# Kernel optimization log

Measured on AMD Instinct MI355X. Metric: run time of the kernel, lower is better.

The kernel has to match this reference:

```python
import jax, jax.numpy as jnp
import numpy as np
from jax import lax

T, B = 128, 256          # rollout length x num envs
H, W, C = 7, 7, 3        # minigrid obs
HID = 128                # lstm hidden
NA = 7                   # actions
NFLAT = 64 * 4 * 4       # conv flatten (7->6->5->4)


def setup_inputs() -> dict:
    key = jax.random.key(0)
    ks = jax.random.split(key, 20)
    N = T * B
    obs = jax.random.randint(ks[0], (N, H, W, C), 0, 11).astype(jnp.float32)
    done = (jax.random.uniform(ks[1], (N,)) < 0.05).astype(jnp.float32)
    h0 = jnp.zeros((1, B, HID), jnp.float32)
    c0 = jnp.zeros((1, B, HID), jnp.float32)
    s = 0.1
    conv1_w = jax.random.normal(ks[2], (16, C, 2, 2)) * s
    conv1_b = jnp.zeros((16,), jnp.float32)
    conv2_w = jax.random.normal(ks[3], (32, 16, 2, 2)) * s
    conv2_b = jnp.zeros((32,), jnp.float32)
    conv3_w = jax.random.normal(ks[4], (64, 32, 2, 2)) * s
    conv3_b = jnp.zeros((64,), jnp.float32)
    w_ih = jax.random.normal(ks[5], (4 * HID, NFLAT)) * 0.03
    w_hh = jax.random.normal(ks[6], (4 * HID, HID)) * 0.08
    b_ih = jnp.zeros((4 * HID,), jnp.float32)
    b_hh = jnp.zeros((4 * HID,), jnp.float32)
    actor_w = jax.random.normal(ks[7], (NA, HID)) * 0.01
    actor_b = jnp.zeros((NA,), jnp.float32)
    critic_w = jax.random.normal(ks[8], (1, HID)) * 0.08
    critic_b = jnp.zeros((1,), jnp.float32)
    return dict(obs=obs, done=done, h0=h0, c0=c0,
                conv1_w=conv1_w, conv1_b=conv1_b,
                conv2_w=conv2_w, conv2_b=conv2_b,
                conv3_w=conv3_w, conv3_b=conv3_b,
                w_ih=w_ih, w_hh=w_hh, b_ih=b_ih, b_hh=b_hh,
                actor_w=actor_w, actor_b=actor_b,
                critic_w=critic_w, critic_b=critic_b)


def _conv(x, w, b):
    # x: [N, Cin, h, w], w: [Cout, Cin, 2, 2], VALID, stride 1
    y = lax.conv_general_dilated(x, w, (1, 1), 'VALID',
                                 dimension_numbers=('NCHW', 'OIHW', 'NCHW'))
    return jax.nn.relu(y + b[None, :, None, None])


def reference(obs, done, h0, c0,
              conv1_w, conv1_b, conv2_w, conv2_b, conv3_w, conv3_b,
              w_ih, w_hh, b_ih, b_hh, actor_w, actor_b, critic_w, critic_b):
    N = obs.shape[0]
    x = jnp.transpose(obs, (0, 3, 1, 2))            # NHWC -> NCHW
    x = _conv(x, conv1_w, conv1_b)
    x = _conv(x, conv2_w, conv2_b)
    x = _conv(x, conv3_w, conv3_b)
    feat = x.reshape(N, -1)                          # [T*B, 1024]

    nb = h0.shape[1]
    xs = feat.reshape(-1, nb, feat.shape[-1])        # [T, B, 1024]
    ds = done.reshape(-1, nb)                        # [T, B]
    bias = b_ih + b_hh

    def step(carry, inp):
        h, c = carry                                  # [B, HID]
        x_t, d_t = inp
        m = (1.0 - d_t)[:, None]
        h = m * h
        c = m * c
        gates = x_t @ w_ih.T + h @ w_hh.T + bias      # [B, 4*HID]
        i, f, g, o = jnp.split(gates, 4, axis=-1)     # torch gate order i,f,g,o
        i = jax.nn.sigmoid(i)
        f = jax.nn.sigmoid(f)
        g = jnp.tanh(g)
        o = jax.nn.sigmoid(o)
        c = f * c + i * g
        h = o * jnp.tanh(c)
        return (h, c), h

    (hT, cT), hs = lax.scan(step, (h0[0], c0[0]), (xs, ds))
    hid = hs.reshape(N, -1)                           # [T*B, HID]
    logits = hid @ actor_w.T + actor_b                # [T*B, NA]
    value = hid @ critic_w.T + critic_b               # [T*B, 1]
    out = jnp.concatenate([logits, value], axis=-1)   # [T*B, NA+1]
    return out, hT[None], cT[None]
```

## Files before the change

### kernel.cpp

```cpp
#include <hip/hip_runtime.h>
#include <hip/hip_bf16.h>


#define N_IMG   32768
#define T_LEN   128
#define B_ENV   256
#define HID     128

typedef _Float16 f16x8 __attribute__((ext_vector_type(8)));
typedef _Float16 f16x2 __attribute__((ext_vector_type(2)));
typedef float    f32x4 __attribute__((ext_vector_type(4)));
typedef unsigned short ushort8v __attribute__((ext_vector_type(8)));
typedef unsigned short ushort4v __attribute__((ext_vector_type(4)));

__device__ __forceinline__ float sigm_(float x) { return 1.0f / (1.0f + __expf(-x)); }
__device__ __forceinline__ float tanh_(float x) { return 2.0f / (1.0f + __expf(-2.0f * x)) - 1.0f; }

__device__ __forceinline__ unsigned short f2h(float x) {
    _Float16 h = (_Float16)x;
    union { _Float16 h; unsigned short u; } un; un.h = h;
    return un.u;
}

#if defined(__has_builtin)
#if __has_builtin(__builtin_amdgcn_fdot2)
#define HAVE_FDOT2 1
#endif
#endif

__device__ __forceinline__ float dot2_(f16x2 a, f16x2 b, float c) {
#ifdef HAVE_FDOT2
    return __builtin_amdgcn_fdot2(a, b, c, false);
#else
    c = fmaf((float)a[0], (float)b[0], c);
    return fmaf((float)a[1], (float)b[1], c);
#endif
}

#define GLDS16(g, l) __builtin_amdgcn_global_load_lds( \
    (const __attribute__((address_space(1))) unsigned int*)(g), \
    (__attribute__((address_space(3))) unsigned int*)(l), 16, 0, 0)

__global__ void prep_wih(const float* __restrict__ w, unsigned short* __restrict__ wb)
{
    const int idx = blockIdx.x * 256 + threadIdx.x;
    const int n = idx >> 10, kk = idx & 1023;
    const int p = kk >> 6, co = kk & 63;
    wb[idx] = f2h(w[n * 1024 + co * 16 + p]);
}

__global__ void prep_convw(const float* __restrict__ w2, const float* __restrict__ w3,
                           unsigned short* __restrict__ wb2g, unsigned short* __restrict__ wb3g)
{
    const int t = blockIdx.x * 256 + threadIdx.x;
    if (t < 2048) {
        const int j = t & 7, lane = (t >> 3) & 63, f = t >> 9;
        const int ky = f >> 1, ct = f & 1;
        const int k = ((lane >> 4) << 3) + j, kx = k >> 4, ci = k & 15;
        wb2g[t] = f2h(w2[(ct * 16 + (lane & 15)) * 64 + ci * 4 + ky * 2 + kx]);
    } else if (t < 10240) {
        const int u = t - 2048;
        const int j = u & 7, lane = (u >> 3) & 63, f = u >> 9;
        const int ct = f >> 2, pos = f & 3;
        const int ci = ((lane >> 4) << 3) + j;
        wb3g[u] = f2h(w3[(ct * 16 + (lane & 15)) * 128 + ci * 4 + pos]);
    }
}

__global__ void prep_whh16(const float* __restrict__ w_hh, unsigned short* __restrict__ whh16)
{
    const int idx = blockIdx.x * 256 + threadIdx.x;
    whh16[idx] = f2h(w_hh[idx]);
}

__global__ __launch_bounds__(256, 2) void conv_fused(
    const float* __restrict__ obs,
    const float* __restrict__ w1, const float* __restrict__ b1,
    const float* __restrict__ b2, const float* __restrict__ b3,
    const unsigned short* __restrict__ wb2g,
    const unsigned short* __restrict__ wb3g,
    unsigned short* __restrict__ featb)
{
    __shared__ __align__(16) unsigned char u1[25856];
    __shared__ __align__(16) unsigned char u2[33024];
    __shared__ float w1s[192];
    __shared__ float b1s[16];

    float* s_obs = (float*)u1;
    unsigned short* c2s = (unsigned short*)u1;
    unsigned short* c1s = (unsigned short*)u2;
    unsigned short* c3s = (unsigned short*)u2;

    const int tid = threadIdx.x, lane = tid & 63, wv = tid >> 6;
    const int base = blockIdx.x * 16;

    if (tid < 192) w1s[tid] = w1[tid];
    if (tid < 16)  b1s[tid] = b1[tid];
    for (int i = tid; i < 16 * 147; i += 256) {
        const int im = i / 147, r = i - im * 147;
        s_obs[im * 148 + r] = obs[(size_t)(base + im) * 147 + r];
    }
    __syncthreads();

    {
        const int img = tid & 15;
        const float* ob = &s_obs[img * 148];
        for (int p = tid >> 4; p < 36; p += 16) {
            const int py = p / 6, px = p % 6;
            float o[12];
#pragma unroll
            for (int ky = 0; ky < 2; ky++)
#pragma unroll
                for (int kx = 0; kx < 2; kx++)
#pragma unroll
                    for (int cc = 0; cc < 3; cc++)
                        o[cc * 4 + ky * 2 + kx] = ob[((py + ky) * 7 + px + kx) * 3 + cc];
            unsigned short res[16];
#pragma unroll
            for (int ci = 0; ci < 16; ci++) {
                float a = b1s[ci];
#pragma unroll
                for (int q = 0; q < 12; q++) a = fmaf(o[q], w1s[ci * 12 + q], a);
                res[ci] = f2h(fmaxf(a, 0.0f));
            }
            *(ushort8v*)&c1s[img * 584 + p * 16]     = *(ushort8v*)&res[0];
            *(ushort8v*)&c1s[img * 584 + p * 16 + 8] = *(ushort8v*)&res[8];
        }
    }
    __syncthreads();

    {
        const int ct = wv & 1, par = wv >> 1;
        const int img = lane & 15, kq = lane >> 4;
        f16x8 wA[2];
        wA[0] = *(const f16x8*)&wb2g[(0 + ct) * 512 + lane * 8];
        wA[1] = *(const f16x8*)&wb2g[(2 + ct) * 512 + lane * 8];
        const float4 b2v = *(const float4*)&b2[ct * 16 + kq * 4];
#pragma unroll 2
        for (int p = par; p < 25; p += 2) {
            const int py = p / 5, px = p % 5;
            f32x4 acc = {0.f, 0.f, 0.f, 0.f};
#pragma unroll
            for (int ky = 0; ky < 2; ky++) {
                const int pix = (py + ky) * 6 + px + (kq >> 1);
                const f16x8 bv = *(const f16x8*)&c1s[img * 584 + pix * 16 + (kq & 1) * 8];
                acc = __builtin_amdgcn_mfma_f32_16x16x32_f16(wA[ky], bv, acc, 0, 0, 0);
            }
            unsigned short r4[4];
            r4[0] = f2h(fmaxf(acc[0] + b2v.x, 0.0f));
            r4[1] = f2h(fmaxf(acc[1] + b2v.y, 0.0f));
            r4[2] = f2h(fmaxf(acc[2] + b2v.z, 0.0f));
            r4[3] = f2h(fmaxf(acc[3] + b2v.w, 0.0f));
            *(ushort4v*)&c2s[img * 808 + p * 32 + ct * 16 + kq * 4] = *(ushort4v*)&r4[0];
        }
    }
    __syncthreads();

    {
        const int ct = wv;
        const int img = lane & 15, kq = lane >> 4;
        f16x8 wA3[4];
#pragma unroll
        for (int pos = 0; pos < 4; pos++)
            wA3[pos] = *(const f16x8*)&wb3g[(ct * 4 + pos) * 512 + lane * 8];
        const float4 b3v = *(const float4*)&b3[ct * 16 + kq * 4];
#pragma unroll 4
        for (int p = 0; p < 16; p++) {
            const int py = p >> 2, px = p & 3;
            f32x4 acc = {0.f, 0.f, 0.f, 0.f};
#pragma unroll
            for (int pos = 0; pos < 4; pos++) {
                const int pix = (py + (pos >> 1)) * 5 + px + (pos & 1);
                const f16x8 bv = *(const f16x8*)&c2s[img * 808 + pix * 32 + kq * 8];
                acc = __builtin_amdgcn_mfma_f32_16x16x32_f16(wA3[pos], bv, acc, 0, 0, 0);
            }
            unsigned short r4[4];
            r4[0] = f2h(fmaxf(acc[0] + b3v.x, 0.0f));
            r4[1] = f2h(fmaxf(acc[1] + b3v.y, 0.0f));
            r4[2] = f2h(fmaxf(acc[2] + b3v.z, 0.0f));
            r4[3] = f2h(fmaxf(acc[3] + b3v.w, 0.0f));
            *(ushort4v*)&c3s[img * 1032 + p * 64 + ct * 16 + kq * 4] = *(ushort4v*)&r4[0];
        }
    }
    __syncthreads();

#pragma unroll
    for (int i = 0; i < 8; i++) {
        const int gi = i * 2048 + tid * 8;
        const int img = gi >> 10, flat = gi & 1023;
        *(ushort8v*)&featb[(size_t)(base + img) * 1024 + flat] =
            *(const ushort8v*)&c3s[img * 1032 + flat];
    }
}

__global__ __launch_bounds__(256, 2) void gemm_xproj_mfma(
    const unsigned short* __restrict__ A,
    const unsigned short* __restrict__ W,
    float* __restrict__ C)
{
    __shared__ unsigned short As[128 * 32];
    __shared__ unsigned short Bs[128 * 32];

    const int tid  = threadIdx.x;
    const int bx = blockIdx.x & 3;
    const int by = blockIdx.x >> 2;
    const int m0 = by * 128, n0 = bx * 128;
    const int lane = tid & 63, wave = tid >> 6;
    const int wm = (wave >> 1) * 64, wn = (wave & 1) * 64;
    const int srow = tid >> 2, sseg = tid & 3;

    const unsigned short* Ag = A + (size_t)(m0 + srow) * 1024 + sseg * 8;
    const unsigned short* Wg = W + (size_t)(n0 + srow) * 1024 + sseg * 8;

    f32x4 acc[4][4];
#pragma unroll
    for (int i = 0; i < 4; i++)
#pragma unroll
        for (int j = 0; j < 4; j++) acc[i][j] = (f32x4){0.f, 0.f, 0.f, 0.f};

    const int fr = lane & 15, fq = lane >> 4;

    for (int k0 = 0; k0 < 1024; k0 += 32) {
        __syncthreads();
        GLDS16(Ag + k0,             (char*)As + tid * 16);
        GLDS16(Ag + k0 + 64 * 1024, (char*)As + tid * 16 + 4096);
        GLDS16(Wg + k0,             (char*)Bs + tid * 16);
        GLDS16(Wg + k0 + 64 * 1024, (char*)Bs + tid * 16 + 4096);
        __syncthreads();

        f16x8 af[4], bfv[4];
#pragma unroll
        for (int i = 0; i < 4; i++)
            af[i] = *(const f16x8*)&As[(wm + i * 16 + fr) * 32 + fq * 8];
#pragma unroll
        for (int j = 0; j < 4; j++)
            bfv[j] = *(const f16x8*)&Bs[(wn + j * 16 + fr) * 32 + fq * 8];
#pragma unroll
        for (int i = 0; i < 4; i++)
#pragma unroll
            for (int j = 0; j < 4; j++)
                acc[i][j] = __builtin_amdgcn_mfma_f32_16x16x32_f16(af[i], bfv[j], acc[i][j], 0, 0, 0);
    }

    const int cr = fq * 4, cc = fr;
#pragma unroll
    for (int i = 0; i < 4; i++) {
#pragma unroll
        for (int j = 0; j < 4; j++) {
            float* cp = &C[(size_t)(m0 + wm + i * 16 + cr) * 512 + (n0 + wn + j * 16 + cc)];
#pragma unroll
            for (int r = 0; r < 4; r++)
                cp[(size_t)r * 512] = acc[i][j][r];
        }
    }
}

__global__ __launch_bounds__(1024, 4) void lstm_dot2(
    const float* __restrict__ xproj, const float* __restrict__ done,
    const float* __restrict__ h0, const float* __restrict__ c0,
    const unsigned short* __restrict__ whh16,
    const float* __restrict__ b_ih, const float* __restrict__ b_hh,
    float* __restrict__ hid, float* __restrict__ out)
{
    const int b   = blockIdx.x;
    const int tid = threadIdx.x;
    const int j   = tid >> 1;
    const int hf  = tid & 1;

    __shared__ __align__(16) _Float16 h_s[HID];
    __shared__ float a_s[512];

    f16x8 w8[8];
    {
        const unsigned short* wrow = whh16 + (size_t)j * 128 + hf * 64;
#pragma unroll
        for (int i = 0; i < 8; i++) w8[i] = *(const f16x8*)&wrow[i * 8];
    }
    const float bias = b_ih[j] + b_hh[j];

    float h = 0.0f, c = 0.0f;
    if (tid < HID) { h = h0[b * HID + tid]; c = c0[b * HID + tid]; }

    float xp   = xproj[(size_t)b * 512 + j];
    float dcur = done[b];

    for (int t = 0; t < T_LEN; t++) {
        if (tid < HID) {
            const float m = 1.0f - dcur;
            h *= m; c *= m;
            h_s[tid] = (_Float16)h;
        }
        __syncthreads();

        const int tn = (t + 1 < T_LEN) ? t + 1 : t;
        const float xpn = xproj[((size_t)tn * B_ENV + b) * 512 + j];
        const float dnn = done[tn * B_ENV + b];

        float a0 = 0.f, a1 = 0.f, a2 = 0.f, a3 = 0.f;
#pragma unroll
        for (int i = 0; i < 8; i++) {
            const f16x8 hv = *(const f16x8*)&h_s[hf * 64 + i * 8];
            a0 = dot2_(__builtin_shufflevector(w8[i], w8[i], 0, 1),
                       __builtin_shufflevector(hv,    hv,    0, 1), a0);
            a1 = dot2_(__builtin_shufflevector(w8[i], w8[i], 2, 3),
                       __builtin_shufflevector(hv,    hv,    2, 3), a1);
            a2 = dot2_(__builtin_shufflevector(w8[i], w8[i], 4, 5),
                       __builtin_shufflevector(hv,    hv,    4, 5), a2);
            a3 = dot2_(__builtin_shufflevector(w8[i], w8[i], 6, 7),
                       __builtin_shufflevector(hv,    hv,    6, 7), a3);
        }
        float g = (a0 + a1) + (a2 + a3);
        g += __shfl_xor(g, 1);
        g += bias + xp;

        const float a = (j >= 256 && j < 384) ? tanh_(g) : sigm_(g);
        if (hf == 0) a_s[j] = a;
        __syncthreads();

        if (tid < HID) {
            const float ig = a_s[tid], fg = a_s[tid + 128];
            const float gg = a_s[tid + 256], og = a_s[tid + 384];
            c = fmaf(fg, c, ig * gg);
            h = og * tanh_(c);
            hid[((size_t)t * B_ENV + b) * HID + tid] = h;
        }

        xp   = xpn;
        dcur = dnn;
    }

    if (tid < HID) {
        out[262144 + b * HID + tid] = h;
        out[294912 + b * HID + tid] = c;
    }
}

__global__ __launch_bounds__(256, 2) void heads_kernel(
    const float* __restrict__ hid,
    const float* __restrict__ aw, const float* __restrict__ ab,
    const float* __restrict__ cw, const float* __restrict__ cb,
    float* __restrict__ out)
{
    __shared__ float hs[32 * 129];
    __shared__ float ws[8 * 130];
    __shared__ float bs[8];

    const int tid = threadIdx.x;
    const int n0 = blockIdx.x * 32;

    for (int i = tid; i < 1024; i += 256) {
        const int r = i >> 7, k = i & 127;
        ws[r * 130 + k] = (r < 7) ? aw[r * 128 + k] : cw[k];
    }
    if (tid < 8) bs[tid] = (tid < 7) ? ab[tid] : cb[0];
    for (int i = tid; i < 4096; i += 256) {
        const int r = i >> 7, k = i & 127;
        hs[r * 129 + k] = hid[(size_t)(n0 + r) * 128 + k];
    }
    __syncthreads();

    const int r = tid >> 3, jj = tid & 7;
    float acc = bs[jj];
    const float* hp = &hs[r * 129];
    const float* wp = &ws[jj * 130];
#pragma unroll
    for (int k = 0; k < 128; k++) acc = fmaf(hp[k], wp[k], acc);
    out[(size_t)(n0 + r) * 8 + jj] = acc;
}

extern "C" void kernel_launch(void* const* d_in, const int* in_sizes, int n_in,
                              void* d_out, int out_size, void* d_ws, size_t ws_size,
                              hipStream_t stream)
{
    (void)in_sizes; (void)n_in; (void)out_size; (void)ws_size;

    const float* obs  = (const float*)d_in[0];
    const float* done = (const float*)d_in[1];
    const float* h0   = (const float*)d_in[2];
    const float* c0   = (const float*)d_in[3];
    const float* w1   = (const float*)d_in[4];
    const float* b1   = (const float*)d_in[5];
    const float* w2   = (const float*)d_in[6];
    const float* b2   = (const float*)d_in[7];
    const float* w3   = (const float*)d_in[8];
    const float* b3   = (const float*)d_in[9];
    const float* w_ih = (const float*)d_in[10];
    const float* w_hh = (const float*)d_in[11];
    const float* b_ih = (const float*)d_in[12];
    const float* b_hh = (const float*)d_in[13];
    const float* aw   = (const float*)d_in[14];
    const float* ab   = (const float*)d_in[15];
    const float* cw   = (const float*)d_in[16];
    const float* cb   = (const float*)d_in[17];
    float* out = (float*)d_out;

    unsigned short* featb = (unsigned short*)d_ws;
    unsigned short* wb    = featb + 33554432ull;
    unsigned short* wb2g  = wb    + 524288ull;
    unsigned short* wb3g  = wb2g  + 2048ull;
    float* xproj = (float*)(wb3g + 8192ull + 2048ull);
    float* hid   = xproj + 16777216ull;
    unsigned short* whh16 = (unsigned short*)(hid + 4194304ull);

    prep_wih<<<2048, 256, 0, stream>>>(w_ih, wb);
    prep_convw<<<40, 256, 0, stream>>>(w2, w3, wb2g, wb3g);
    prep_whh16<<<256, 256, 0, stream>>>(w_hh, whh16);
    conv_fused<<<2048, 256, 0, stream>>>(obs, w1, b1, b2, b3, wb2g, wb3g, featb);
    gemm_xproj_mfma<<<1024, 256, 0, stream>>>(featb, wb, xproj);
    lstm_dot2<<<256, 1024, 0, stream>>>(xproj, done, h0, c0, whh16, b_ih, b_hh, hid, out);
    heads_kernel<<<1024, 256, 0, stream>>>(hid, aw, ab, cw, cb, out);
}
```

Before: 333.0 us.

## Restructure LSTM recurrence with butterfly gate reduction and double-buffered hidden state

The LSTM kernel now uses 512 threads per environment, four per hidden unit. Each thread computes partial dot products for all four gates over a 32-wide slice, and a butterfly of xor shuffles leaves each lane holding one full gate pre-activation. Every thread then computes the cell update redundantly, so the gate activations no longer go through shared memory, and with a double-buffered h only one barrier per timestep is needed instead of two. The W_ih rows are permuted in prep so xproj comes out gate-interleaved per hidden unit, and W_hh is repacked to match. The cost is more registers per thread and redundant transcendental work on every lane.

```diff
diff --git a/kernel.cpp b/kernel.cpp
--- a/kernel.cpp
+++ b/kernel.cpp
@@ -12,6 +12,8 @@
 typedef float    f32x4 __attribute__((ext_vector_type(4)));
 typedef unsigned short ushort8v __attribute__((ext_vector_type(8)));
 typedef unsigned short ushort4v __attribute__((ext_vector_type(4)));
+
+union f16x8_pairs { f16x8 v; f16x2 p[4]; };
 
 __device__ __forceinline__ float sigm_(float x) { return 1.0f / (1.0f + __expf(-x)); }
 __device__ __forceinline__ float tanh_(float x) { return 2.0f / (1.0f + __expf(-2.0f * x)) - 1.0f; }
@@ -44,8 +46,10 @@
 __global__ void prep_wih(const float* __restrict__ w, unsigned short* __restrict__ wb)
 {
     const int idx = blockIdx.x * 256 + threadIdx.x;
-    const int n = idx >> 10, kk = idx & 1023;
+    const int np = idx >> 10, kk = idx & 1023;
     const int p = kk >> 6, co = kk & 63;
+    const int g = np & 3, ci = np >> 2;
+    const int n = g * 128 + ci;
     wb[idx] = f2h(w[n * 1024 + co * 16 + p]);
 }
 
@@ -67,10 +71,13 @@
     }
 }
 
-__global__ void prep_whh16(const float* __restrict__ w_hh, unsigned short* __restrict__ whh16)
+__global__ void prep_whhr(const float* __restrict__ w_hh, unsigned short* __restrict__ whhr)
 {
     const int idx = blockIdx.x * 256 + threadIdx.x;
-    whh16[idx] = f2h(w_hh[idx]);
+    const int thr = idx >> 7, r = idx & 127;
+    const int g = r >> 5, k = r & 31;
+    const int ci = thr >> 2, s = thr & 3;
+    whhr[idx] = f2h(w_hh[(g * 128 + ci) * 128 + s * 32 + k]);
 }
 
 __global__ __launch_bounds__(256, 2) void conv_fused(
@@ -255,83 +262,91 @@
     }
 }
 
-__global__ __launch_bounds__(1024, 4) void lstm_dot2(
+__global__ __launch_bounds__(512, 2) void lstm_bfly(
     const float* __restrict__ xproj, const float* __restrict__ done,
     const float* __restrict__ h0, const float* __restrict__ c0,
-    const unsigned short* __restrict__ whh16,
+    const unsigned short* __restrict__ whhr,
     const float* __restrict__ b_ih, const float* __restrict__ b_hh,
     float* __restrict__ hid, float* __restrict__ out)
 {
     const int b   = blockIdx.x;
     const int tid = threadIdx.x;
-    const int j   = tid >> 1;
-    const int hf  = tid & 1;
-
-    __shared__ __align__(16) _Float16 h_s[HID];
-    __shared__ float a_s[512];
-
-    f16x8 w8[8];
+    const int ci  = tid >> 2;
+    const int s   = tid & 3;
+
+    __shared__ __align__(16) _Float16 hbuf[2][HID];
+
+    f16x8_pairs w[4][4];
     {
-        const unsigned short* wrow = whh16 + (size_t)j * 128 + hf * 64;
-#pragma unroll
-        for (int i = 0; i < 8; i++) w8[i] = *(const f16x8*)&wrow[i * 8];
-    }
-    const float bias = b_ih[j] + b_hh[j];
-
-    float h = 0.0f, c = 0.0f;
-    if (tid < HID) { h = h0[b * HID + tid]; c = c0[b * HID + tid]; }
-
-    float xp   = xproj[(size_t)b * 512 + j];
+        const unsigned short* wp = whhr + (size_t)tid * 128;
+#pragma unroll
+        for (int g = 0; g < 4; g++)
+#pragma unroll
+            for (int i = 0; i < 4; i++)
+                w[g][i].v = *(const f16x8*)&wp[g * 32 + i * 8];
+    }
+    const float bias_l = b_ih[s * 128 + ci] + b_hh[s * 128 + ci];
+
+    float c = c0[b * HID + ci];
+    float h = h0[b * HID + ci];
     float dcur = done[b];
 
+    if (tid < HID)
+        hbuf[0][tid] = (_Float16)(h0[b * HID + tid] * (1.0f - dcur));
+
+    float xq = bias_l + xproj[(size_t)b * 512 + ci * 4 + s];
+    __syncthreads();
+
+    int p = 0;
     for (int t = 0; t < T_LEN; t++) {
-        if (tid < HID) {
-            const float m = 1.0f - dcur;
-            h *= m; c *= m;
-            h_s[tid] = (_Float16)h;
-        }
+        const int tn = (t + 1 < T_LEN) ? t + 1 : t;
+        const float xqn = bias_l + xproj[((size_t)tn * B_ENV + b) * 512 + ci * 4 + s];
+        const float dnn = done[tn * B_ENV + b];
+
+        f16x8_pairs hv[4];
+#pragma unroll
+        for (int i = 0; i < 4; i++)
+            hv[i].v = *(const f16x8*)&hbuf[p][s * 32 + i * 8];
+
+        float a0 = (s == 0) ? xq : 0.0f;
+        float a1 = (s == 1) ? xq : 0.0f;
+        float a2 = (s == 2) ? xq : 0.0f;
+        float a3 = (s == 3) ? xq : 0.0f;
+#pragma unroll
+        for (int i = 0; i < 4; i++) {
+#pragma unroll
+            for (int pr = 0; pr < 4; pr++) {
+                const f16x2 hp = hv[i].p[pr];
+                a0 = dot2_(w[0][i].p[pr], hp, a0);
+                a1 = dot2_(w[1][i].p[pr], hp, a1);
+                a2 = dot2_(w[2][i].p[pr], hp, a2);
+                a3 = dot2_(w[3][i].p[pr], hp, a3);
+            }
+        }
+
+        a0 += __shfl_xor(a0, 1); a1 += __shfl_xor(a1, 1);
+        a2 += __shfl_xor(a2, 2); a3 += __shfl_xor(a3, 2);
+        a0 += __shfl_xor(a0, 2); a1 += __shfl_xor(a1, 2);
+        a2 += __shfl_xor(a2, 1); a3 += __shfl_xor(a3, 1);
+
+        const float gi = sigm_(a0), gf = sigm_(a1);
+        const float gg = tanh_(a2), go = sigm_(a3);
+        const float m = 1.0f - dcur;
+        c = fmaf(gf, c * m, gi * gg);
+        h = go * tanh_(c);
+
+        if (s == 0) {
+            hid[((size_t)t * B_ENV + b) * HID + ci] = h;
+            hbuf[p ^ 1][ci] = (_Float16)(h * (1.0f - dnn));
+        }
+
+        xq = xqn; dcur = dnn; p ^= 1;
         __syncthreads();
-
-        const int tn = (t + 1 < T_LEN) ? t + 1 : t;
-        const float xpn = xproj[((size_t)tn * B_ENV + b) * 512 + j];
-        const float dnn = done[tn * B_ENV + b];
-
-        float a0 = 0.f, a1 = 0.f, a2 = 0.f, a3 = 0.f;
-#pragma unroll
-        for (int i = 0; i < 8; i++) {
-            const f16x8 hv = *(const f16x8*)&h_s[hf * 64 + i * 8];
-            a0 = dot2_(__builtin_shufflevector(w8[i], w8[i], 0, 1),
-                       __builtin_shufflevector(hv,    hv,    0, 1), a0);
-            a1 = dot2_(__builtin_shufflevector(w8[i], w8[i], 2, 3),
-                       __builtin_shufflevector(hv,    hv,    2, 3), a1);
-            a2 = dot2_(__builtin_shufflevector(w8[i], w8[i], 4, 5),
-                       __builtin_shufflevector(hv,    hv,    4, 5), a2);
-            a3 = dot2_(__builtin_shufflevector(w8[i], w8[i], 6, 7),
-                       __builtin_shufflevector(hv,    hv,    6, 7), a3);
-        }
-        float g = (a0 + a1) + (a2 + a3);
-        g += __shfl_xor(g, 1);
-        g += bias + xp;
-
-        const float a = (j >= 256 && j < 384) ? tanh_(g) : sigm_(g);
-        if (hf == 0) a_s[j] = a;
-        __syncthreads();
-
-        if (tid < HID) {
-            const float ig = a_s[tid], fg = a_s[tid + 128];
-            const float gg = a_s[tid + 256], og = a_s[tid + 384];
-            c = fmaf(fg, c, ig * gg);
-            h = og * tanh_(c);
-            hid[((size_t)t * B_ENV + b) * HID + tid] = h;
-        }
-
-        xp   = xpn;
-        dcur = dnn;
-    }
-
-    if (tid < HID) {
-        out[262144 + b * HID + tid] = h;
-        out[294912 + b * HID + tid] = c;
+    }
+
+    if (s == 0) {
+        out[262144 + b * HID + ci] = h;
+        out[294912 + b * HID + ci] = c;
     }
 }
 
@@ -400,13 +415,13 @@
     unsigned short* wb3g  = wb2g  + 2048ull;
     float* xproj = (float*)(wb3g + 8192ull + 2048ull);
     float* hid   = xproj + 16777216ull;
-    unsigned short* whh16 = (unsigned short*)(hid + 4194304ull);
+    unsigned short* whhr = (unsigned short*)(hid + 4194304ull);
 
     prep_wih<<<2048, 256, 0, stream>>>(w_ih, wb);
     prep_convw<<<40, 256, 0, stream>>>(w2, w3, wb2g, wb3g);
-    prep_whh16<<<256, 256, 0, stream>>>(w_hh, whh16);
+    prep_whhr<<<256, 256, 0, stream>>>(w_hh, whhr);
     conv_fused<<<2048, 256, 0, stream>>>(obs, w1, b1, b2, b3, wb2g, wb3g, featb);
     gemm_xproj_mfma<<<1024, 256, 0, stream>>>(featb, wb, xproj);
-    lstm_dot2<<<256, 1024, 0, stream>>>(xproj, done, h0, c0, whh16, b_ih, b_hh, hid, out);
+    lstm_bfly<<<256, 512, 0, stream>>>(xproj, done, h0, c0, whhr, b_ih, b_hh, hid, out);
     heads_kernel<<<1024, 256, 0, stream>>>(hid, aw, ab, cw, cb, out);
 }
```

Result: faster. 314.8 us (-5.5%).
